# Kernel tuning notes

Measured on AMD Instinct MI355X. Metric: run time of the kernel, lower is better.

The kernel has to match this reference:

```python
import jax, jax.numpy as jnp
import numpy as np

BATCH = 2048
IN_DIM = 4096
OUT_DIM = 1024
N_EDGES = 16384  # mat_wann.connection_count
CONSTANT_WEIGHT = 1.0


def setup_inputs() -> dict:
    key = jax.random.key(0)
    k1, k2, k3 = jax.random.split(key, 3)
    x = jax.random.normal(k1, (BATCH, IN_DIM), dtype=jnp.float32)
    # one scalar Linear(1,1,bias=False) per connection, all init to constant_weight
    weights = jnp.ones((N_EDGES,), dtype=jnp.float32) * CONSTANT_WEIGHT
    # edge list: src input column, dst output node (sorted => segment-friendly)
    edge_src = jax.random.randint(k2, (N_EDGES,), 0, IN_DIM, dtype=jnp.int32)
    edge_dst = jnp.sort(jax.random.randint(k3, (N_EDGES,), 0, OUT_DIM, dtype=jnp.int32))
    return {"x": x, "weights": weights, "edge_src": edge_src, "edge_dst": edge_dst}


def reference(x, weights, edge_src, edge_dst):
    # gather per-edge input column and apply the per-edge scalar linear
    contrib = x[:, edge_src] * weights[None, :]              # [B, E]
    # scatter-add (segment-reduce) per-edge contributions into output nodes
    node_sums = jax.ops.segment_sum(contrib.T, edge_dst, num_segments=OUT_DIM)  # [OUT_DIM, B]
    # per-node activation (self.activations[...]); nodes with no incoming edges
    # stay zero, matching torch.zeros for empty rows since tanh(0)=0
    h = jnp.tanh(node_sums.T)                                 # [B, OUT_DIM]
    # activation_list applied to concatenated outputs
    return jax.nn.sigmoid(h)
```

## Files before the change

kernel.cpp:

```cpp
#include <hip/hip_runtime.h>
#include <hip/hip_fp16.h>
#include <math.h>

#define BATCH   2048
#define IN_DIM  4096
#define OUT_DIM 1024
#define N_EDGES 16384

#define R    4
#define NG   16
#define LCAP 64


__device__ __forceinline__ float hbits_to_f(unsigned int u) {
    __half_raw r; r.x = (unsigned short)u;
    return __half2float(r);
}

__device__ __forceinline__ float act(float a) {
    const float e2 = __expf(2.0f * a);
    const float h = 1.0f - 2.0f / (e2 + 1.0f);
    return 1.0f / (1.0f + __expf(-h));
}

__global__ __launch_bounds__(256) void prep_kernel(
        const int* __restrict__ edge_dst,
        const int* __restrict__ edge_src,
        const float* __restrict__ weights,
        uint4* __restrict__ rec4,
        int* __restrict__ gm8arr) {
    __shared__ int s_lo[64], s_deg[64], s_gm;
    const int g = blockIdx.x, t = threadIdx.x, l = t & 63;
    if (t == 0) s_gm = 8;
    __syncthreads();
    if (t < 64) {
        const int n = g * 64 + l;
        int lo = 0, hi = N_EDGES;
        while (lo < hi) { int m = (lo + hi) >> 1; if (edge_dst[m] < n) lo = m + 1; else hi = m; }
        int lo2 = lo, hi2 = N_EDGES;
        while (lo2 < hi2) { int m = (lo2 + hi2) >> 1; if (edge_dst[m] < n + 1) lo2 = m + 1; else hi2 = m; }
        int deg = lo2 - lo; if (deg > LCAP) deg = LCAP;
        s_lo[l] = lo; s_deg[l] = deg;
        atomicMax(&s_gm, deg);
    }
    __syncthreads();
    const int gm8 = (s_gm + 7) & ~7;
    if (t == 0) gm8arr[g] = gm8;
    const int lo = s_lo[l], deg = s_deg[l];
    const int nch = gm8 >> 2;
    for (int c = t >> 6; c < nch; c += 4) {
        unsigned int v[4];
#pragma unroll
        for (int k = 0; k < 4; k++) {
            const int i = c * 4 + k;
            unsigned int p = 0;
            if (i < deg) {
                const int e = lo + i;
                const __half hw = __float2half(weights[e]);
                p = (unsigned int)edge_src[e] |
                    ((unsigned int)__half_as_ushort(hw) << 16);
            }
            v[k] = p;
        }
        rec4[(size_t)(g * (LCAP / 4) + c) * 64 + l] =
            make_uint4(v[0], v[1], v[2], v[3]);
    }
}

#define PROC(q)                                                            \
    {                                                                      \
        { const unsigned int u = (q).x; const float4 xv = xs[u & 0xFFFFu]; \
          const float wv = hbits_to_f(u >> 16);                            \
          b0 = fmaf(wv, xv.x, b0); b1 = fmaf(wv, xv.y, b1);                \
          b2 = fmaf(wv, xv.z, b2); b3 = fmaf(wv, xv.w, b3); }              \
        { const unsigned int u = (q).y; const float4 xv = xs[u & 0xFFFFu]; \
          const float wv = hbits_to_f(u >> 16);                            \
          b0 = fmaf(wv, xv.x, b0); b1 = fmaf(wv, xv.y, b1);                \
          b2 = fmaf(wv, xv.z, b2); b3 = fmaf(wv, xv.w, b3); }              \
        { const unsigned int u = (q).z; const float4 xv = xs[u & 0xFFFFu]; \
          const float wv = hbits_to_f(u >> 16);                            \
          b0 = fmaf(wv, xv.x, b0); b1 = fmaf(wv, xv.y, b1);                \
          b2 = fmaf(wv, xv.z, b2); b3 = fmaf(wv, xv.w, b3); }              \
        { const unsigned int u = (q).w; const float4 xv = xs[u & 0xFFFFu]; \
          const float wv = hbits_to_f(u >> 16);                            \
          b0 = fmaf(wv, xv.x, b0); b1 = fmaf(wv, xv.y, b1);                \
          b2 = fmaf(wv, xv.z, b2); b3 = fmaf(wv, xv.w, b3); }              \
    }

__global__ __launch_bounds__(512, 4) void fused_kernel(
        const float* __restrict__ x,
        const uint4* __restrict__ rec4,
        const int* __restrict__ gm8arr,
        float* __restrict__ out) {
    __shared__ float4 xs[IN_DIM];

    const int brow = blockIdx.x * R;
    const int t = threadIdx.x;
    const int w = t >> 6, l = t & 63;

    const int g0 = 2 * w, g1 = 2 * w + 1;
    const uint4* ep0 = rec4 + (size_t)(g0 * (LCAP / 4)) * 64 + l;
    const uint4* ep1 = rec4 + (size_t)(g1 * (LCAP / 4)) * 64 + l;

    uint4 q0a = ep0[0], q0b = ep0[64];
    uint4 q1a = ep1[0], q1b = ep1[64];
    const int nch0 = __builtin_amdgcn_readfirstlane(gm8arr[g0]) >> 2;
    const int nch1 = __builtin_amdgcn_readfirstlane(gm8arr[g1]) >> 2;

    const float* xr = x + (size_t)brow * IN_DIM;
#pragma unroll
    for (int k = 0; k < IN_DIM / 512; k++) {
        const int c = t + k * 512;
        xs[c] = make_float4(xr[c], xr[IN_DIM + c],
                            xr[2 * IN_DIM + c], xr[3 * IN_DIM + c]);
    }
    __syncthreads();

    {
        float b0 = 0.0f, b1 = 0.0f, b2 = 0.0f, b3 = 0.0f;
        uint4 qa = q0a, qb = q0b;
        for (int c = 0; c + 2 < nch0; c += 2) {
            const uint4 qc = ep0[(c + 2) * 64];
            const uint4 qd = ep0[(c + 3) * 64];
            PROC(qa); PROC(qb);
            qa = qc; qb = qd;
        }
        PROC(qa); PROC(qb);
        const int node = g0 * 64 + l;
        out[(size_t)(brow + 0) * OUT_DIM + node] = act(b0);
        out[(size_t)(brow + 1) * OUT_DIM + node] = act(b1);
        out[(size_t)(brow + 2) * OUT_DIM + node] = act(b2);
        out[(size_t)(brow + 3) * OUT_DIM + node] = act(b3);
    }
    {
        float b0 = 0.0f, b1 = 0.0f, b2 = 0.0f, b3 = 0.0f;
        uint4 qa = q1a, qb = q1b;
        for (int c = 0; c + 2 < nch1; c += 2) {
            const uint4 qc = ep1[(c + 2) * 64];
            const uint4 qd = ep1[(c + 3) * 64];
            PROC(qa); PROC(qb);
            qa = qc; qb = qd;
        }
        PROC(qa); PROC(qb);
        const int node = g1 * 64 + l;
        out[(size_t)(brow + 0) * OUT_DIM + node] = act(b0);
        out[(size_t)(brow + 1) * OUT_DIM + node] = act(b1);
        out[(size_t)(brow + 2) * OUT_DIM + node] = act(b2);
        out[(size_t)(brow + 3) * OUT_DIM + node] = act(b3);
    }
}

extern "C" void kernel_launch(void* const* d_in, const int* in_sizes, int n_in,
                              void* d_out, int out_size, void* d_ws, size_t ws_size,
                              hipStream_t stream) {
    const float* x        = (const float*)d_in[0];
    const float* weights  = (const float*)d_in[1];
    const int*   edge_src = (const int*)d_in[2];
    const int*   edge_dst = (const int*)d_in[3];
    float*       out      = (float*)d_out;

    uint4* rec4   = (uint4*)d_ws;
    int*   gm8arr = (int*)((char*)d_ws +
                           (size_t)NG * (LCAP / 4) * 64 * sizeof(uint4));

    prep_kernel<<<NG, 256, 0, stream>>>(edge_dst, edge_src, weights,
                                        rec4, gm8arr);

    fused_kernel<<<BATCH / R, 512, 0, stream>>>(x, rec4, gm8arr, out);
}
```

Measured before the change: 95.47 us.

## Sort output nodes by degree to balance groups and stage coalesced output stores

A new single-block prep kernel counting-sorts the output nodes by in-degree, so each 64-lane group holds nodes of similar degree. This cuts the padded edge slots that every lane must process up to the group maximum, and padding is now rounded to multiples of 4 instead of 8. Each wave pairs a heavy group with a light one to balance work across waves. Results are permuted back through LDS and written with coalesced float4 stores. The cost is an extra kernel launch and an extra sync. The gmaxarr atomicMax also relies on workspace contents that are never zeroed.

```diff
diff --git a/kernel.cpp b/kernel.cpp
--- a/kernel.cpp
+++ b/kernel.cpp
@@ -23,32 +23,51 @@
     return 1.0f / (1.0f + __expf(-h));
 }
 
-__global__ __launch_bounds__(256) void prep_kernel(
+__global__ __launch_bounds__(1024) void sortprep_kernel(
         const int* __restrict__ edge_dst,
+        int2* __restrict__ nodeinfo,
+        int* __restrict__ colmap,
+        int* __restrict__ gmaxarr) {
+    __shared__ int hist[LCAP + 1], tail[LCAP + 1];
+    const int n = threadIdx.x;
+    if (n <= LCAP) { hist[n] = 0; tail[n] = 0; }
+    __syncthreads();
+    int lo = 0, hi = N_EDGES;
+    while (lo < hi) { int m = (lo + hi) >> 1; if (edge_dst[m] < n) lo = m + 1; else hi = m; }
+    int lo2 = lo, hi2 = N_EDGES;
+    while (lo2 < hi2) { int m = (lo2 + hi2) >> 1; if (edge_dst[m] < n + 1) lo2 = m + 1; else hi2 = m; }
+    int deg = lo2 - lo; if (deg > LCAP) deg = LCAP;
+    nodeinfo[n] = make_int2(lo, deg);
+    atomicAdd(&hist[deg], 1);
+    __syncthreads();
+    if (n == 0) {
+        int run = 0;
+        for (int d = LCAP; d >= 0; d--) { int c = hist[d]; hist[d] = run; run += c; }
+    }
+    __syncthreads();
+    const int rank = hist[deg] + atomicAdd(&tail[deg], 1);
+    colmap[rank] = n;
+    atomicMax(&gmaxarr[rank >> 6], deg);
+}
+
+__global__ __launch_bounds__(256) void scatter_kernel(
+        const int2* __restrict__ nodeinfo,
+        const int* __restrict__ colmap,
         const int* __restrict__ edge_src,
         const float* __restrict__ weights,
         uint4* __restrict__ rec4,
-        int* __restrict__ gm8arr) {
-    __shared__ int s_lo[64], s_deg[64], s_gm;
+        const int* __restrict__ gmaxarr,
+        int* __restrict__ gm4arr) {
     const int g = blockIdx.x, t = threadIdx.x, l = t & 63;
-    if (t == 0) s_gm = 8;
-    __syncthreads();
-    if (t < 64) {
-        const int n = g * 64 + l;
-        int lo = 0, hi = N_EDGES;
-        while (lo < hi) { int m = (lo + hi) >> 1; if (edge_dst[m] < n) lo = m + 1; else hi = m; }
-        int lo2 = lo, hi2 = N_EDGES;
-        while (lo2 < hi2) { int m = (lo2 + hi2) >> 1; if (edge_dst[m] < n + 1) lo2 = m + 1; else hi2 = m; }
-        int deg = lo2 - lo; if (deg > LCAP) deg = LCAP;
-        s_lo[l] = lo; s_deg[l] = deg;
-        atomicMax(&s_gm, deg);
-    }
-    __syncthreads();
-    const int gm8 = (s_gm + 7) & ~7;
-    if (t == 0) gm8arr[g] = gm8;
-    const int lo = s_lo[l], deg = s_deg[l];
-    const int nch = gm8 >> 2;
-    for (int c = t >> 6; c < nch; c += 4) {
+    const int gm = gmaxarr[g];
+    int gm4 = (gm + 3) & ~3; if (gm4 < 8) gm4 = 8;
+    if (t == 0) gm4arr[g] = gm4;
+    const int nch  = gm4 >> 2;
+    const int nchw = (nch + 1) & ~1;
+    const int n = colmap[g * 64 + l];
+    const int2 info = nodeinfo[n];
+    const int lo = info.x, deg = info.y;
+    for (int c = t >> 6; c < nchw; c += 4) {
         unsigned int v[4];
 #pragma unroll
         for (int k = 0; k < 4; k++) {
@@ -87,10 +106,27 @@
           b2 = fmaf(wv, xv.z, b2); b3 = fmaf(wv, xv.w, b3); }              \
     }
 
+#define RUN_GROUP(ep, nch, qa_in, qb_in, A0, A1, A2, A3)                   \
+    {                                                                      \
+        float b0 = 0.0f, b1 = 0.0f, b2 = 0.0f, b3 = 0.0f;                  \
+        uint4 qa = qa_in, qb = qb_in;                                      \
+        int c = 0;                                                         \
+        for (; c + 2 < nch; c += 2) {                                      \
+            const uint4 qc = ep[(c + 2) * 64];                             \
+            const uint4 qd = ep[(c + 3) * 64];                             \
+            PROC(qa); PROC(qb);                                            \
+            qa = qc; qb = qd;                                              \
+        }                                                                  \
+        PROC(qa);                                                          \
+        if (c + 1 < nch) PROC(qb);                                         \
+        A0 = b0; A1 = b1; A2 = b2; A3 = b3;                                \
+    }
+
 __global__ __launch_bounds__(512, 4) void fused_kernel(
         const float* __restrict__ x,
         const uint4* __restrict__ rec4,
-        const int* __restrict__ gm8arr,
+        const int* __restrict__ gm4arr,
+        const int* __restrict__ colmap,
         float* __restrict__ out) {
     __shared__ float4 xs[IN_DIM];
 
@@ -98,14 +134,16 @@
     const int t = threadIdx.x;
     const int w = t >> 6, l = t & 63;
 
-    const int g0 = 2 * w, g1 = 2 * w + 1;
+    const int g0 = w, g1 = (NG - 1) - w;
     const uint4* ep0 = rec4 + (size_t)(g0 * (LCAP / 4)) * 64 + l;
     const uint4* ep1 = rec4 + (size_t)(g1 * (LCAP / 4)) * 64 + l;
 
     uint4 q0a = ep0[0], q0b = ep0[64];
     uint4 q1a = ep1[0], q1b = ep1[64];
-    const int nch0 = __builtin_amdgcn_readfirstlane(gm8arr[g0]) >> 2;
-    const int nch1 = __builtin_amdgcn_readfirstlane(gm8arr[g1]) >> 2;
+    const int col0 = colmap[g0 * 64 + l];
+    const int col1 = colmap[g1 * 64 + l];
+    const int nch0 = __builtin_amdgcn_readfirstlane(gm4arr[g0]) >> 2;
+    const int nch1 = __builtin_amdgcn_readfirstlane(gm4arr[g1]) >> 2;
 
     const float* xr = x + (size_t)brow * IN_DIM;
 #pragma unroll
@@ -116,37 +154,28 @@
     }
     __syncthreads();
 
-    {
-        float b0 = 0.0f, b1 = 0.0f, b2 = 0.0f, b3 = 0.0f;
-        uint4 qa = q0a, qb = q0b;
-        for (int c = 0; c + 2 < nch0; c += 2) {
-            const uint4 qc = ep0[(c + 2) * 64];
-            const uint4 qd = ep0[(c + 3) * 64];
-            PROC(qa); PROC(qb);
-            qa = qc; qb = qd;
-        }
-        PROC(qa); PROC(qb);
-        const int node = g0 * 64 + l;
-        out[(size_t)(brow + 0) * OUT_DIM + node] = act(b0);
-        out[(size_t)(brow + 1) * OUT_DIM + node] = act(b1);
-        out[(size_t)(brow + 2) * OUT_DIM + node] = act(b2);
-        out[(size_t)(brow + 3) * OUT_DIM + node] = act(b3);
-    }
-    {
-        float b0 = 0.0f, b1 = 0.0f, b2 = 0.0f, b3 = 0.0f;
-        uint4 qa = q1a, qb = q1b;
-        for (int c = 0; c + 2 < nch1; c += 2) {
-            const uint4 qc = ep1[(c + 2) * 64];
-            const uint4 qd = ep1[(c + 3) * 64];
-            PROC(qa); PROC(qb);
-            qa = qc; qb = qd;
-        }
-        PROC(qa); PROC(qb);
-        const int node = g1 * 64 + l;
-        out[(size_t)(brow + 0) * OUT_DIM + node] = act(b0);
-        out[(size_t)(brow + 1) * OUT_DIM + node] = act(b1);
-        out[(size_t)(brow + 2) * OUT_DIM + node] = act(b2);
-        out[(size_t)(brow + 3) * OUT_DIM + node] = act(b3);
+    float a00, a01, a02, a03, a10, a11, a12, a13;
+    RUN_GROUP(ep0, nch0, q0a, q0b, a00, a01, a02, a03);
+    RUN_GROUP(ep1, nch1, q1a, q1b, a10, a11, a12, a13);
+
+    __syncthreads();
+    float* sacc = (float*)xs;
+    sacc[0 * OUT_DIM + col0] = act(a00);
+    sacc[1 * OUT_DIM + col0] = act(a01);
+    sacc[2 * OUT_DIM + col0] = act(a02);
+    sacc[3 * OUT_DIM + col0] = act(a03);
+    sacc[0 * OUT_DIM + col1] = act(a10);
+    sacc[1 * OUT_DIM + col1] = act(a11);
+    sacc[2 * OUT_DIM + col1] = act(a12);
+    sacc[3 * OUT_DIM + col1] = act(a13);
+    __syncthreads();
+    const float4* sv = (const float4*)sacc;
+#pragma unroll
+    for (int k = 0; k < (R * OUT_DIM / 4) / 512; k++) {
+        const int i = t + k * 512;
+        const int row = i >> (10 - 2);
+        const int c4 = (i & (OUT_DIM / 4 - 1)) * 4;
+        *(float4*)(out + (size_t)(brow + row) * OUT_DIM + c4) = sv[i];
     }
 }
 
@@ -159,12 +188,17 @@
     const int*   edge_dst = (const int*)d_in[3];
     float*       out      = (float*)d_out;
 
-    uint4* rec4   = (uint4*)d_ws;
-    int*   gm8arr = (int*)((char*)d_ws +
-                           (size_t)NG * (LCAP / 4) * 64 * sizeof(uint4));
-
-    prep_kernel<<<NG, 256, 0, stream>>>(edge_dst, edge_src, weights,
-                                        rec4, gm8arr);
-
-    fused_kernel<<<BATCH / R, 512, 0, stream>>>(x, rec4, gm8arr, out);
-}
+    char* p = (char*)d_ws;
+    uint4* rec4     = (uint4*)p;            p += (size_t)NG * (LCAP / 4) * 64 * sizeof(uint4);
+    int*   gmaxarr  = (int*)p;              p += NG * sizeof(int);
+    int*   gm4arr   = (int*)p;              p += NG * sizeof(int);
+    int*   colmap   = (int*)p;              p += OUT_DIM * sizeof(int);
+    int2*  nodeinfo = (int2*)p;
+
+    sortprep_kernel<<<1, 1024, 0, stream>>>(edge_dst, nodeinfo, colmap, gmaxarr);
+
+    scatter_kernel<<<NG, 256, 0, stream>>>(nodeinfo, colmap, edge_src, weights,
+                                           rec4, gmaxarr, gm4arr);
+
+    fused_kernel<<<BATCH / R, 512, 0, stream>>>(x, rec4, gm4arr, colmap, out);
+}
```

Measured after the change: 101.2 us. 1.06x slower.

## Stage x in LDS as packed bf16 and pad edge chunks to multiples of four

Applied to the files above, without the earlier changes.

Converts the staged input rows to bf16 and packs four batch rows into a uint2, which halves LDS footprint and gather bandwidth. This could allow more blocks per CU and cheaper LDS reads. Edge records now hold a pre-scaled byte offset, and the per-group edge count is padded to a multiple of 4 instead of 8, so fewer zero-padding records are processed. Quantising x to bf16 lowers accumulation precision and may loosen agreement with the float32 reference.

```diff
diff --git a/kernel.cpp b/kernel.cpp
--- a/kernel.cpp
+++ b/kernel.cpp
@@ -17,6 +17,11 @@
     return __half2float(r);
 }
 
+__device__ __forceinline__ unsigned int f_to_bf16(float f) {
+    unsigned int u = __float_as_uint(f);
+    return (u + 0x7FFFu + ((u >> 16) & 1u)) >> 16;
+}
+
 __device__ __forceinline__ float act(float a) {
     const float e2 = __expf(2.0f * a);
     const float h = 1.0f - 2.0f / (e2 + 1.0f);
@@ -28,7 +33,7 @@
         const int* __restrict__ edge_src,
         const float* __restrict__ weights,
         uint4* __restrict__ rec4,
-        int* __restrict__ gm8arr) {
+        int* __restrict__ gm4arr) {
     __shared__ int s_lo[64], s_deg[64], s_gm;
     const int g = blockIdx.x, t = threadIdx.x, l = t & 63;
     if (t == 0) s_gm = 8;
@@ -44,11 +49,12 @@
         atomicMax(&s_gm, deg);
     }
     __syncthreads();
-    const int gm8 = (s_gm + 7) & ~7;
-    if (t == 0) gm8arr[g] = gm8;
+    const int gm4 = (s_gm + 3) & ~3;
+    if (t == 0) gm4arr[g] = gm4;
+    const int nch  = gm4 >> 2;
+    const int nchw = (nch + 1) & ~1;
     const int lo = s_lo[l], deg = s_deg[l];
-    const int nch = gm8 >> 2;
-    for (int c = t >> 6; c < nch; c += 4) {
+    for (int c = t >> 6; c < nchw; c += 4) {
         unsigned int v[4];
 #pragma unroll
         for (int k = 0; k < 4; k++) {
@@ -57,7 +63,7 @@
             if (i < deg) {
                 const int e = lo + i;
                 const __half hw = __float2half(weights[e]);
-                p = (unsigned int)edge_src[e] |
+                p = ((unsigned int)edge_src[e] << 3) |
                     ((unsigned int)__half_as_ushort(hw) << 16);
             }
             v[k] = p;
@@ -67,32 +73,39 @@
     }
 }
 
-#define PROC(q)                                                            \
+#define SLOT(u)                                                            \
     {                                                                      \
-        { const unsigned int u = (q).x; const float4 xv = xs[u & 0xFFFFu]; \
-          const float wv = hbits_to_f(u >> 16);                            \
-          b0 = fmaf(wv, xv.x, b0); b1 = fmaf(wv, xv.y, b1);                \
-          b2 = fmaf(wv, xv.z, b2); b3 = fmaf(wv, xv.w, b3); }              \
-        { const unsigned int u = (q).y; const float4 xv = xs[u & 0xFFFFu]; \
-          const float wv = hbits_to_f(u >> 16);                            \
-          b0 = fmaf(wv, xv.x, b0); b1 = fmaf(wv, xv.y, b1);                \
-          b2 = fmaf(wv, xv.z, b2); b3 = fmaf(wv, xv.w, b3); }              \
-        { const unsigned int u = (q).z; const float4 xv = xs[u & 0xFFFFu]; \
-          const float wv = hbits_to_f(u >> 16);                            \
-          b0 = fmaf(wv, xv.x, b0); b1 = fmaf(wv, xv.y, b1);                \
-          b2 = fmaf(wv, xv.z, b2); b3 = fmaf(wv, xv.w, b3); }              \
-        { const unsigned int u = (q).w; const float4 xv = xs[u & 0xFFFFu]; \
-          const float wv = hbits_to_f(u >> 16);                            \
-          b0 = fmaf(wv, xv.x, b0); b1 = fmaf(wv, xv.y, b1);                \
-          b2 = fmaf(wv, xv.z, b2); b3 = fmaf(wv, xv.w, b3); }              \
+        const uint2 xv = *(const uint2*)((const char*)xs + ((u) & 0xFFF8u));\
+        const float wv = hbits_to_f((u) >> 16);                            \
+        b0 = fmaf(wv, __uint_as_float(xv.x << 16), b0);                    \
+        b1 = fmaf(wv, __uint_as_float(xv.x & 0xFFFF0000u), b1);            \
+        b2 = fmaf(wv, __uint_as_float(xv.y << 16), b2);                    \
+        b3 = fmaf(wv, __uint_as_float(xv.y & 0xFFFF0000u), b3);            \
+    }
+#define PROC(q) { SLOT((q).x); SLOT((q).y); SLOT((q).z); SLOT((q).w); }
+
+#define RUN_GROUP(ep, nch, qa_in, qb_in, A0, A1, A2, A3)                   \
+    {                                                                      \
+        float b0 = 0.0f, b1 = 0.0f, b2 = 0.0f, b3 = 0.0f;                  \
+        uint4 qa = qa_in, qb = qb_in;                                      \
+        int c = 0;                                                         \
+        for (; c + 2 < nch; c += 2) {                                      \
+            const uint4 qc = ep[(c + 2) * 64];                             \
+            const uint4 qd = ep[(c + 3) * 64];                             \
+            PROC(qa); PROC(qb);                                            \
+            qa = qc; qb = qd;                                              \
+        }                                                                  \
+        PROC(qa);                                                          \
+        if (c + 1 < nch) PROC(qb);                                         \
+        A0 = b0; A1 = b1; A2 = b2; A3 = b3;                                \
     }
 
 __global__ __launch_bounds__(512, 4) void fused_kernel(
         const float* __restrict__ x,
         const uint4* __restrict__ rec4,
-        const int* __restrict__ gm8arr,
+        const int* __restrict__ gm4arr,
         float* __restrict__ out) {
-    __shared__ float4 xs[IN_DIM];
+    __shared__ uint2 xs[IN_DIM];
 
     const int brow = blockIdx.x * R;
     const int t = threadIdx.x;
@@ -104,50 +117,34 @@
 
     uint4 q0a = ep0[0], q0b = ep0[64];
     uint4 q1a = ep1[0], q1b = ep1[64];
-    const int nch0 = __builtin_amdgcn_readfirstlane(gm8arr[g0]) >> 2;
-    const int nch1 = __builtin_amdgcn_readfirstlane(gm8arr[g1]) >> 2;
+    const int nch0 = __builtin_amdgcn_readfirstlane(gm4arr[g0]) >> 2;
+    const int nch1 = __builtin_amdgcn_readfirstlane(gm4arr[g1]) >> 2;
 
     const float* xr = x + (size_t)brow * IN_DIM;
 #pragma unroll
     for (int k = 0; k < IN_DIM / 512; k++) {
         const int c = t + k * 512;
-        xs[c] = make_float4(xr[c], xr[IN_DIM + c],
-                            xr[2 * IN_DIM + c], xr[3 * IN_DIM + c]);
+        const unsigned int r0 = f_to_bf16(xr[c]);
+        const unsigned int r1 = f_to_bf16(xr[IN_DIM + c]);
+        const unsigned int r2 = f_to_bf16(xr[2 * IN_DIM + c]);
+        const unsigned int r3 = f_to_bf16(xr[3 * IN_DIM + c]);
+        xs[c] = make_uint2((r1 << 16) | r0, (r3 << 16) | r2);
     }
     __syncthreads();
 
-    {
-        float b0 = 0.0f, b1 = 0.0f, b2 = 0.0f, b3 = 0.0f;
-        uint4 qa = q0a, qb = q0b;
-        for (int c = 0; c + 2 < nch0; c += 2) {
-            const uint4 qc = ep0[(c + 2) * 64];
-            const uint4 qd = ep0[(c + 3) * 64];
-            PROC(qa); PROC(qb);
-            qa = qc; qb = qd;
-        }
-        PROC(qa); PROC(qb);
-        const int node = g0 * 64 + l;
-        out[(size_t)(brow + 0) * OUT_DIM + node] = act(b0);
-        out[(size_t)(brow + 1) * OUT_DIM + node] = act(b1);
-        out[(size_t)(brow + 2) * OUT_DIM + node] = act(b2);
-        out[(size_t)(brow + 3) * OUT_DIM + node] = act(b3);
-    }
-    {
-        float b0 = 0.0f, b1 = 0.0f, b2 = 0.0f, b3 = 0.0f;
-        uint4 qa = q1a, qb = q1b;
-        for (int c = 0; c + 2 < nch1; c += 2) {
-            const uint4 qc = ep1[(c + 2) * 64];
-            const uint4 qd = ep1[(c + 3) * 64];
-            PROC(qa); PROC(qb);
-            qa = qc; qb = qd;
-        }
-        PROC(qa); PROC(qb);
-        const int node = g1 * 64 + l;
-        out[(size_t)(brow + 0) * OUT_DIM + node] = act(b0);
-        out[(size_t)(brow + 1) * OUT_DIM + node] = act(b1);
-        out[(size_t)(brow + 2) * OUT_DIM + node] = act(b2);
-        out[(size_t)(brow + 3) * OUT_DIM + node] = act(b3);
-    }
+    float a00, a01, a02, a03, a10, a11, a12, a13;
+    RUN_GROUP(ep0, nch0, q0a, q0b, a00, a01, a02, a03);
+    RUN_GROUP(ep1, nch1, q1a, q1b, a10, a11, a12, a13);
+
+    const int node0 = g0 * 64 + l, node1 = g1 * 64 + l;
+    out[(size_t)(brow + 0) * OUT_DIM + node0] = act(a00);
+    out[(size_t)(brow + 1) * OUT_DIM + node0] = act(a01);
+    out[(size_t)(brow + 2) * OUT_DIM + node0] = act(a02);
+    out[(size_t)(brow + 3) * OUT_DIM + node0] = act(a03);
+    out[(size_t)(brow + 0) * OUT_DIM + node1] = act(a10);
+    out[(size_t)(brow + 1) * OUT_DIM + node1] = act(a11);
+    out[(size_t)(brow + 2) * OUT_DIM + node1] = act(a12);
+    out[(size_t)(brow + 3) * OUT_DIM + node1] = act(a13);
 }
 
 extern "C" void kernel_launch(void* const* d_in, const int* in_sizes, int n_in,
@@ -160,11 +157,11 @@
     float*       out      = (float*)d_out;
 
     uint4* rec4   = (uint4*)d_ws;
-    int*   gm8arr = (int*)((char*)d_ws +
+    int*   gm4arr = (int*)((char*)d_ws +
                            (size_t)NG * (LCAP / 4) * 64 * sizeof(uint4));
 
     prep_kernel<<<NG, 256, 0, stream>>>(edge_dst, edge_src, weights,
-                                        rec4, gm8arr);
+                                        rec4, gm4arr);
 
-    fused_kernel<<<BATCH / R, 512, 0, stream>>>(x, rec4, gm8arr, out);
+    fused_kernel<<<BATCH / R, 512, 0, stream>>>(x, rec4, gm4arr, out);
 }
```

Result: no change. 95.88 us (median of 2 runs) (+0.4%).
